# Performance work log

Hardware: AMD Instinct MI355X
Metric: run time of the kernel (lower is better)

## Reference

```python
import jax, jax.numpy as jnp
import numpy as np

B, N, QD = 2, 4096, 512
HEADS, DIM_HEAD = 8, 64
INNER = HEADS * DIM_HEAD  # 512
SCALE = DIM_HEAD ** -0.5


def setup_inputs() -> dict:
    key = jax.random.key(0)
    ks = jax.random.split(key, 6)
    s = 0.02
    return {
        "x": jax.random.normal(ks[0], (B, N, QD), dtype=jnp.float32),
        "Wq": jax.random.normal(ks[1], (QD, INNER), dtype=jnp.float32) * s,
        "Wk": jax.random.normal(ks[2], (QD, INNER), dtype=jnp.float32) * s,
        "Wv": jax.random.normal(ks[3], (QD, INNER), dtype=jnp.float32) * s,
        "Wo": jax.random.normal(ks[4], (INNER, QD), dtype=jnp.float32) * s,
        "bo": jnp.zeros((QD,), dtype=jnp.float32),
    }


def reference(x, Wq, Wk, Wv, Wo, bo):
    # self-attention: context = x; mask = None; attention_sf = False
    q = x @ Wq  # [B, N, INNER]
    k = x @ Wk
    v = x @ Wv
    # split heads: [B, H, N, D]
    def split(t):
        return t.reshape(B, N, HEADS, DIM_HEAD).transpose(0, 2, 1, 3)
    q, k, v = split(q), split(k), split(v)
    # fp32 QK^T (ATTN_PRECISION='fp32' path)
    sim = jnp.einsum('bhid,bhjd->bhij', q.astype(jnp.float32), k.astype(jnp.float32)) * SCALE
    attn = jax.nn.softmax(sim, axis=-1)
    out = jnp.einsum('bhij,bhjd->bhid', attn, v)  # [B, H, N, D]
    out = out.transpose(0, 2, 1, 3).reshape(B, N, INNER)
    return out @ Wo + bo  # Dropout(p=0) is identity
```

## Files before the change

### kernel.cpp

```cpp
#include <hip/hip_runtime.h>
#include <hip/hip_bf16.h>


typedef __attribute__((ext_vector_type(8))) short short8;
typedef __attribute__((ext_vector_type(4))) float floatx4;

#define MFMA16(a, b, c) __builtin_amdgcn_mfma_f32_16x16x32_bf16((a), (b), (c), 0, 0, 0)

static __device__ __forceinline__ unsigned short f2b(float f) {
  unsigned int u = __float_as_uint(f);
  u += 0x7FFFu + ((u >> 16) & 1u);
  return (unsigned short)(u >> 16);
}

static __device__ __forceinline__ unsigned int pkb(float a, float b) {
  float2 t{a, b};
  __hip_bfloat162 h = __float22bfloat162_rn(t);
  union { __hip_bfloat162 h2; unsigned int u; } cv;
  cv.h2 = h;
  return cv.u;
}

__global__ __launch_bounds__(256) void wt_cvt_kernel(
    const float* __restrict__ Wq, const float* __restrict__ Wk,
    const float* __restrict__ Wv, const float* __restrict__ Wo,
    unsigned short* __restrict__ wtq, unsigned short* __restrict__ wtk,
    unsigned short* __restrict__ wtv, unsigned short* __restrict__ wto) {
  const int z = blockIdx.z;
  const float* __restrict__ W = (z == 0) ? Wq : (z == 1) ? Wk : (z == 2) ? Wv : Wo;
  unsigned short* __restrict__ T = (z == 0) ? wtq : (z == 1) ? wtk : (z == 2) ? wtv : wto;
  const int k0 = blockIdx.x * 32, c0 = blockIdx.y * 32;
  __shared__ float Ts[32][33];
  const int tid = threadIdx.x;
  const int r = tid >> 3, cc = (tid & 7) * 4;
  const float4 v = *(const float4*)(W + (k0 + r) * 512 + c0 + cc);
  Ts[r][cc] = v.x; Ts[r][cc + 1] = v.y; Ts[r][cc + 2] = v.z; Ts[r][cc + 3] = v.w;
  __syncthreads();
  const unsigned long long uu =
      (unsigned long long)pkb(Ts[cc][r], Ts[cc + 1][r]) |
      ((unsigned long long)pkb(Ts[cc + 2][r], Ts[cc + 3][r]) << 32);
  *(unsigned long long*)(T + (c0 + r) * 512 + k0 + cc) = uu;
}

__global__ __launch_bounds__(256) void qkv_proj_kernel(
    const float* __restrict__ x, const unsigned short* __restrict__ wtq,
    const unsigned short* __restrict__ wtk,
    const unsigned short* __restrict__ wtv, unsigned short* __restrict__ qo,
    unsigned short* __restrict__ ko, unsigned short* __restrict__ vo) {
  const int z = blockIdx.z;
  const unsigned short* __restrict__ wt = (z == 0) ? wtq : (z == 1) ? wtk : wtv;
  const int m0 = blockIdx.x * 128;
  const int c0 = blockIdx.y * 128;
  __shared__ __align__(16) unsigned short As[128 * 40];
  __shared__ __align__(16) unsigned short Bs[128 * 40];
  const int tid = threadIdx.x;
  const int lane = tid & 63, wvid = tid >> 6;
  const int i = lane & 15, q = lane >> 4;
  const int wy = wvid >> 1, wx = wvid & 1;
  const int arow = tid >> 1, ch = (tid & 1) * 16;
  floatx4 acc[4][4] = {};
  for (int k0 = 0; k0 < 512; k0 += 32) {
    __syncthreads();
    {
      const float* src = x + (m0 + arow) * 512 + k0 + ch;
      unsigned int av[8];
#pragma unroll
      for (int j = 0; j < 8; ++j) av[j] = pkb(src[2 * j], src[2 * j + 1]);
      *(short8*)&As[arow * 40 + ch] = *(short8*)&av[0];
      *(short8*)&As[arow * 40 + ch + 8] = *(short8*)&av[4];
      const unsigned short* bs = wt + (c0 + arow) * 512 + k0 + ch;
      *(short8*)&Bs[arow * 40 + ch] = *(const short8*)(bs);
      *(short8*)&Bs[arow * 40 + ch + 8] = *(const short8*)(bs + 8);
    }
    __syncthreads();
    short8 af[4], bfr[4];
#pragma unroll
    for (int t = 0; t < 4; ++t)
      af[t] = *(const short8*)&As[(wy * 64 + t * 16 + i) * 40 + q * 8];
#pragma unroll
    for (int g = 0; g < 4; ++g)
      bfr[g] = *(const short8*)&Bs[(wx * 64 + g * 16 + i) * 40 + q * 8];
#pragma unroll
    for (int t = 0; t < 4; ++t)
#pragma unroll
      for (int g = 0; g < 4; ++g) acc[t][g] = MFMA16(af[t], bfr[g], acc[t][g]);
  }
#pragma unroll
  for (int t = 0; t < 4; ++t)
#pragma unroll
    for (int g = 0; g < 4; ++g) {
      const int col = c0 + wx * 64 + g * 16 + i;
      const int h = col >> 6, d = col & 63;
      const int row0 = m0 + wy * 64 + t * 16 + q * 4;
      const int b = row0 >> 12;
      const int n0 = row0 & 4095;
      if (z == 2) {
        unsigned int* dst =
            (unsigned int*)&vo[(((b * 8 + h) * 64 + d) << 12) + n0];
        dst[0] = pkb(acc[t][g][0], acc[t][g][1]);
        dst[1] = pkb(acc[t][g][2], acc[t][g][3]);
      } else {
        unsigned short* dst = (z == 0) ? qo : ko;
        const float sc = (z == 0) ? 0.125f : 1.0f;
#pragma unroll
        for (int r = 0; r < 4; ++r)
          dst[(((b * 8 + h) << 12) + (n0 + r)) * 64 + d] =
              f2b(acc[t][g][r] * sc);
      }
    }
}

__global__ __launch_bounds__(256, 4) void flash_kernel(
    const unsigned short* __restrict__ Q, const unsigned short* __restrict__ K,
    const unsigned short* __restrict__ Vt, unsigned short* __restrict__ O) {
  const int bh = blockIdx.x;
  const int m0 = blockIdx.y * 128;
  const int tid = threadIdx.x;
  const int lane = tid & 63, w = tid >> 6;
  const int i = lane & 15, q = lane >> 4;
  const unsigned short* qp = Q + bh * (4096 * 64);
  const unsigned short* kp = K + bh * (4096 * 64);
  const unsigned short* vp = Vt + bh * (64 * 4096);

  __shared__ __align__(16) unsigned short Ks[64 * 72];
  __shared__ __align__(16) unsigned short Vs[64 * 72];
  __shared__ __align__(16) unsigned short Ps[4][32 * 72];

  const int srow = tid >> 3;
  const int scol = (tid & 7) * 8;
  const unsigned short* kg = kp + srow * 64 + scol;
  const unsigned short* vg = vp + srow * 4096 + scol;

  short8 qf[2][2];
#pragma unroll
  for (int t = 0; t < 2; ++t)
#pragma unroll
    for (int kc = 0; kc < 2; ++kc)
      qf[t][kc] = *(const short8*)(qp + (m0 + w * 32 + t * 16 + i) * 64 +
                                   kc * 32 + q * 8);

  floatx4 accO[2][4] = {};
  floatx4 accL[2] = {};
  short8 ones;
  {
    const short ov = (i == 0) ? (short)0x3F80 : (short)0;
#pragma unroll
    for (int j = 0; j < 8; ++j) ones[j] = ov;
  }
  const floatx4 zf = {0.f, 0.f, 0.f, 0.f};

  *(short8*)&Ks[srow * 72 + scol] = *(const short8*)(kg);
  *(short8*)&Ks[(srow + 32) * 72 + scol] = *(const short8*)(kg + 32 * 64);
  *(short8*)&Vs[srow * 72 + scol] = *(const short8*)(vg);
  *(short8*)&Vs[(srow + 32) * 72 + scol] = *(const short8*)(vg + 32 * 4096);
  __syncthreads();

  unsigned short* pw = &Ps[w][0];
  for (int jt = 0; jt < 64; ++jt) {
    short8 kn0, kn1, vn0, vn1;
    if (jt < 63) {
      kn0 = *(const short8*)(kg + (jt + 1) * 4096);
      kn1 = *(const short8*)(kg + (jt + 1) * 4096 + 32 * 64);
      vn0 = *(const short8*)(vg + (jt + 1) * 64);
      vn1 = *(const short8*)(vg + (jt + 1) * 64 + 32 * 4096);
    }
#pragma unroll
    for (int g = 0; g < 4; ++g) {
      const short8 kf0 = *(const short8*)(&Ks[(g * 16 + i) * 72 + q * 8]);
      const short8 kf1 = *(const short8*)(&Ks[(g * 16 + i) * 72 + 32 + q * 8]);
#pragma unroll
      for (int t = 0; t < 2; ++t) {
        floatx4 s = MFMA16(kf0, qf[t][0], zf);
        s = MFMA16(kf1, qf[t][1], s);
        const float e0 = __expf(s[0]), e1 = __expf(s[1]);
        const float e2 = __expf(s[2]), e3 = __expf(s[3]);
        *(unsigned long long*)&pw[(t * 16 + i) * 72 + g * 16 + q * 4] =
            (unsigned long long)pkb(e0, e1) |
            ((unsigned long long)pkb(e2, e3) << 32);
      }
    }
    short8 pf[2][2];
#pragma unroll
    for (int t = 0; t < 2; ++t) {
      pf[t][0] = *(const short8*)(pw + (t * 16 + i) * 72 + q * 8);
      pf[t][1] = *(const short8*)(pw + (t * 16 + i) * 72 + 32 + q * 8);
      accL[t] = MFMA16(pf[t][0], ones, accL[t]);
      accL[t] = MFMA16(pf[t][1], ones, accL[t]);
    }
#pragma unroll
    for (int dg = 0; dg < 4; ++dg) {
      const short8 vf0 = *(const short8*)(&Vs[(dg * 16 + i) * 72 + q * 8]);
      const short8 vf1 = *(const short8*)(&Vs[(dg * 16 + i) * 72 + 32 + q * 8]);
#pragma unroll
      for (int t = 0; t < 2; ++t) {
        accO[t][dg] = MFMA16(pf[t][0], vf0, accO[t][dg]);
        accO[t][dg] = MFMA16(pf[t][1], vf1, accO[t][dg]);
      }
    }
    __syncthreads();
    if (jt < 63) {
      *(short8*)&Ks[srow * 72 + scol] = kn0;
      *(short8*)&Ks[(srow + 32) * 72 + scol] = kn1;
      *(short8*)&Vs[srow * 72 + scol] = vn0;
      *(short8*)&Vs[(srow + 32) * 72 + scol] = vn1;
    }
    __syncthreads();
  }

  const int b = bh >> 3, h = bh & 7;
#pragma unroll
  for (int t = 0; t < 2; ++t) {
    float inv[4];
#pragma unroll
    for (int r = 0; r < 4; ++r) {
      const float l = __shfl(accL[t][r], lane & 48, 64);
      inv[r] = 1.0f / l;
    }
#pragma unroll
    for (int dg = 0; dg < 4; ++dg)
#pragma unroll
      for (int r = 0; r < 4; ++r) {
        const int n = m0 + w * 32 + t * 16 + q * 4 + r;
        const int col = h * 64 + dg * 16 + i;
        O[((b << 12) + n) * 512 + col] = f2b(accO[t][dg][r] * inv[r]);
      }
  }
}

__global__ __launch_bounds__(256) void out_proj_kernel(
    const unsigned short* __restrict__ A, const unsigned short* __restrict__ wto,
    const float* __restrict__ bo, float* __restrict__ out) {
  const int m0 = blockIdx.x * 128, c0 = blockIdx.y * 128;
  __shared__ __align__(16) unsigned short As[128 * 40];
  __shared__ __align__(16) unsigned short Bs[128 * 40];
  const int tid = threadIdx.x;
  const int lane = tid & 63, wvid = tid >> 6;
  const int i = lane & 15, q = lane >> 4;
  const int wy = wvid >> 1, wx = wvid & 1;
  const int arow = tid >> 1, ch = (tid & 1) * 16;
  floatx4 acc[4][4] = {};
  for (int k0 = 0; k0 < 512; k0 += 32) {
    __syncthreads();
    {
      const unsigned short* as = A + (m0 + arow) * 512 + k0 + ch;
      *(short8*)&As[arow * 40 + ch] = *(const short8*)(as);
      *(short8*)&As[arow * 40 + ch + 8] = *(const short8*)(as + 8);
      const unsigned short* bs = wto + (c0 + arow) * 512 + k0 + ch;
      *(short8*)&Bs[arow * 40 + ch] = *(const short8*)(bs);
      *(short8*)&Bs[arow * 40 + ch + 8] = *(const short8*)(bs + 8);
    }
    __syncthreads();
    short8 af[4], bfr[4];
#pragma unroll
    for (int t = 0; t < 4; ++t)
      af[t] = *(const short8*)&As[(wy * 64 + t * 16 + i) * 40 + q * 8];
#pragma unroll
    for (int g = 0; g < 4; ++g)
      bfr[g] = *(const short8*)&Bs[(wx * 64 + g * 16 + i) * 40 + q * 8];
#pragma unroll
    for (int t = 0; t < 4; ++t)
#pragma unroll
      for (int g = 0; g < 4; ++g) acc[t][g] = MFMA16(af[t], bfr[g], acc[t][g]);
  }
#pragma unroll
  for (int t = 0; t < 4; ++t)
#pragma unroll
    for (int g = 0; g < 4; ++g) {
      const int col = c0 + wx * 64 + g * 16 + i;
      const float bias = bo[col];
#pragma unroll
      for (int r = 0; r < 4; ++r) {
        const int row = m0 + wy * 64 + t * 16 + q * 4 + r;
        out[row * 512 + col] = acc[t][g][r] + bias;
      }
    }
}

extern "C" void kernel_launch(void* const* d_in, const int* in_sizes, int n_in,
                              void* d_out, int out_size, void* d_ws,
                              size_t ws_size, hipStream_t stream) {
  const float* x = (const float*)d_in[0];
  const float* Wq = (const float*)d_in[1];
  const float* Wk = (const float*)d_in[2];
  const float* Wv = (const float*)d_in[3];
  const float* Wo = (const float*)d_in[4];
  const float* bo = (const float*)d_in[5];
  float* out = (float*)d_out;

  const size_t tsz = (size_t)16 * 4096 * 64;
  unsigned short* qws = (unsigned short*)d_ws;
  unsigned short* kws = qws + tsz;
  unsigned short* vws = kws + tsz;
  unsigned short* ows = vws + tsz;
  unsigned short* wtq = ows + tsz;
  unsigned short* wtk = wtq + 512 * 512;
  unsigned short* wtv = wtk + 512 * 512;
  unsigned short* wto = wtv + 512 * 512;

  wt_cvt_kernel<<<dim3(16, 16, 4), 256, 0, stream>>>(Wq, Wk, Wv, Wo, wtq, wtk,
                                                     wtv, wto);
  qkv_proj_kernel<<<dim3(64, 4, 3), 256, 0, stream>>>(x, wtq, wtk, wtv, qws,
                                                      kws, vws);
  flash_kernel<<<dim3(16, 32), 256, 0, stream>>>(qws, kws, vws, ows);
  out_proj_kernel<<<dim3(64, 4), 256, 0, stream>>>(ows, wto, bo, out);
}
```

Before: 225.5 us.

## Split flash KV range across wave pairs, swizzle LDS, use exp2, shrink out-proj tiles

The flash kernel now takes 64-row query tiles, with pairs of waves splitting each 64-key block into two 32-key halves. The two partial outputs and row sums are combined through shared memory at the end, which doubles the grid and raises occupancy. LDS tiles use XOR swizzles in place of padding, and exp is replaced by exp2 with log2(e) folded into the Q scale. Row sums move from an MFMA with a ones vector to scalar adds plus shuffles. The output projection switches to 64x64 tiles for more blocks, at the cost of less data reuse per tile.

Result: slower. 239.1 us (+6.1%).

```diff
diff --git a/kernel.cpp b/kernel.cpp
--- a/kernel.cpp
+++ b/kernel.cpp
@@ -6,6 +6,14 @@
 typedef __attribute__((ext_vector_type(4))) float floatx4;
 
 #define MFMA16(a, b, c) __builtin_amdgcn_mfma_f32_16x16x32_bf16((a), (b), (c), 0, 0, 0)
+
+#if __has_builtin(__builtin_amdgcn_exp2f)
+#define EXP2(x) __builtin_amdgcn_exp2f(x)
+#else
+#define EXP2(x) exp2f(x)
+#endif
+
+#define QSCALE 0.18033688011112042f
 
 static __device__ __forceinline__ unsigned short f2b(float f) {
   unsigned int u = __float_as_uint(f);
@@ -101,7 +109,7 @@
         dst[1] = pkb(acc[t][g][2], acc[t][g][3]);
       } else {
         unsigned short* dst = (z == 0) ? qo : ko;
-        const float sc = (z == 0) ? 0.125f : 1.0f;
+        const float sc = (z == 0) ? QSCALE : 1.0f;
 #pragma unroll
         for (int r = 0; r < 4; ++r)
           dst[(((b * 8 + h) << 12) + (n0 + r)) * 64 + d] =
@@ -110,101 +118,132 @@
     }
 }
 
-__global__ __launch_bounds__(256, 4) void flash_kernel(
+__global__ __launch_bounds__(256, 5) void flash_kernel(
     const unsigned short* __restrict__ Q, const unsigned short* __restrict__ K,
     const unsigned short* __restrict__ Vt, unsigned short* __restrict__ O) {
-  const int bh = blockIdx.x;
-  const int m0 = blockIdx.y * 128;
+  const int m0 = blockIdx.x * 64;
+  const int bh = blockIdx.y;
   const int tid = threadIdx.x;
   const int lane = tid & 63, w = tid >> 6;
   const int i = lane & 15, q = lane >> 4;
+  const int rt = w & 1;
+  const int kg = w >> 1;
+  const int sl7 = i & 7, sl3 = i & 3;
   const unsigned short* qp = Q + bh * (4096 * 64);
   const unsigned short* kp = K + bh * (4096 * 64);
   const unsigned short* vp = Vt + bh * (64 * 4096);
 
-  __shared__ __align__(16) unsigned short Ks[64 * 72];
-  __shared__ __align__(16) unsigned short Vs[64 * 72];
-  __shared__ __align__(16) unsigned short Ps[4][32 * 72];
-
-  const int srow = tid >> 3;
-  const int scol = (tid & 7) * 8;
-  const unsigned short* kg = kp + srow * 64 + scol;
-  const unsigned short* vg = vp + srow * 4096 + scol;
+  __shared__ __align__(16) unsigned short SM[12288];
+  unsigned short* Ks = SM + kg * 2048;
+  unsigned short* Vs = SM + 4096 + kg * 2048;
+  unsigned short* pw = SM + 8192 + w * 1024;
+
+  const int t128 = tid & 127;
+  const int sr = t128 >> 2;
+  const int sc = t128 & 3;
+  const unsigned short* kgl = kp + (kg * 2048 + sr) * 64 + sc * 8;
+  const int ko1 = sr * 64 + ((sc ^ (sr & 7)) * 8);
+  const int ko2 = sr * 64 + (((sc + 4) ^ (sr & 7)) * 8);
+  const unsigned short* vgl = vp + sr * 4096 + kg * 2048 + sc * 8;
+  const int vo1 = sr * 32 + ((sc ^ (sr & 3)) * 8);
+  const int vo2 = (sr + 32) * 32 + ((sc ^ (sr & 3)) * 8);
 
   short8 qf[2][2];
 #pragma unroll
   for (int t = 0; t < 2; ++t)
 #pragma unroll
     for (int kc = 0; kc < 2; ++kc)
-      qf[t][kc] = *(const short8*)(qp + (m0 + w * 32 + t * 16 + i) * 64 +
+      qf[t][kc] = *(const short8*)(qp + (m0 + rt * 32 + t * 16 + i) * 64 +
                                    kc * 32 + q * 8);
 
   floatx4 accO[2][4] = {};
-  floatx4 accL[2] = {};
-  short8 ones;
-  {
-    const short ov = (i == 0) ? (short)0x3F80 : (short)0;
-#pragma unroll
-    for (int j = 0; j < 8; ++j) ones[j] = ov;
-  }
+  float Lacc[2] = {0.f, 0.f};
   const floatx4 zf = {0.f, 0.f, 0.f, 0.f};
 
-  *(short8*)&Ks[srow * 72 + scol] = *(const short8*)(kg);
-  *(short8*)&Ks[(srow + 32) * 72 + scol] = *(const short8*)(kg + 32 * 64);
-  *(short8*)&Vs[srow * 72 + scol] = *(const short8*)(vg);
-  *(short8*)&Vs[(srow + 32) * 72 + scol] = *(const short8*)(vg + 32 * 4096);
+  *(short8*)&Ks[ko1] = *(const short8*)(kgl);
+  *(short8*)&Ks[ko2] = *(const short8*)(kgl + 32);
+  *(short8*)&Vs[vo1] = *(const short8*)(vgl);
+  *(short8*)&Vs[vo2] = *(const short8*)(vgl + 32 * 4096);
   __syncthreads();
 
-  unsigned short* pw = &Ps[w][0];
   for (int jt = 0; jt < 64; ++jt) {
-    short8 kn0, kn1, vn0, vn1;
-    if (jt < 63) {
-      kn0 = *(const short8*)(kg + (jt + 1) * 4096);
-      kn1 = *(const short8*)(kg + (jt + 1) * 4096 + 32 * 64);
-      vn0 = *(const short8*)(vg + (jt + 1) * 64);
-      vn1 = *(const short8*)(vg + (jt + 1) * 64 + 32 * 4096);
-    }
-#pragma unroll
-    for (int g = 0; g < 4; ++g) {
-      const short8 kf0 = *(const short8*)(&Ks[(g * 16 + i) * 72 + q * 8]);
-      const short8 kf1 = *(const short8*)(&Ks[(g * 16 + i) * 72 + 32 + q * 8]);
+#pragma unroll
+    for (int g = 0; g < 2; ++g) {
+      const short8 kf0 =
+          *(const short8*)&Ks[(g * 16 + i) * 64 + ((q ^ sl7) * 8)];
+      const short8 kf1 =
+          *(const short8*)&Ks[(g * 16 + i) * 64 + (((4 + q) ^ sl7) * 8)];
 #pragma unroll
       for (int t = 0; t < 2; ++t) {
         floatx4 s = MFMA16(kf0, qf[t][0], zf);
         s = MFMA16(kf1, qf[t][1], s);
-        const float e0 = __expf(s[0]), e1 = __expf(s[1]);
-        const float e2 = __expf(s[2]), e3 = __expf(s[3]);
-        *(unsigned long long*)&pw[(t * 16 + i) * 72 + g * 16 + q * 4] =
+        const float e0 = EXP2(s[0]), e1 = EXP2(s[1]);
+        const float e2 = EXP2(s[2]), e3 = EXP2(s[3]);
+        Lacc[t] += (e0 + e1) + (e2 + e3);
+        *(unsigned long long*)&pw[(t * 16 + i) * 32 +
+                                  (((2 * g + (q >> 1)) ^ sl3) * 8) +
+                                  (q & 1) * 4] =
             (unsigned long long)pkb(e0, e1) |
             ((unsigned long long)pkb(e2, e3) << 32);
       }
     }
-    short8 pf[2][2];
+    short8 pf[2];
+#pragma unroll
+    for (int t = 0; t < 2; ++t)
+      pf[t] = *(const short8*)&pw[(t * 16 + i) * 32 + ((q ^ sl3) * 8)];
+#pragma unroll
+    for (int dg = 0; dg < 4; ++dg) {
+      const short8 vfd =
+          *(const short8*)&Vs[(dg * 16 + i) * 32 + ((q ^ sl3) * 8)];
+      accO[0][dg] = MFMA16(pf[0], vfd, accO[0][dg]);
+      accO[1][dg] = MFMA16(pf[1], vfd, accO[1][dg]);
+    }
+    short8 kn0, kn1, vn0, vn1;
+    if (jt < 63) {
+      kn0 = *(const short8*)(kgl + (jt + 1) * 2048);
+      kn1 = *(const short8*)(kgl + (jt + 1) * 2048 + 32);
+      vn0 = *(const short8*)(vgl + (jt + 1) * 32);
+      vn1 = *(const short8*)(vgl + (jt + 1) * 32 + 32 * 4096);
+    }
+    __syncthreads();
+    if (jt < 63) {
+      *(short8*)&Ks[ko1] = kn0;
+      *(short8*)&Ks[ko2] = kn1;
+      *(short8*)&Vs[vo1] = vn0;
+      *(short8*)&Vs[vo2] = vn1;
+    }
+    __syncthreads();
+  }
+
+#pragma unroll
+  for (int t = 0; t < 2; ++t) {
+    Lacc[t] += __shfl_xor(Lacc[t], 16);
+    Lacc[t] += __shfl_xor(Lacc[t], 32);
+  }
+  float* MB = (float*)SM;
+  if (kg == 1) {
+    float* dst = MB + (rt * 64 + lane) * 35;
 #pragma unroll
     for (int t = 0; t < 2; ++t) {
-      pf[t][0] = *(const short8*)(pw + (t * 16 + i) * 72 + q * 8);
-      pf[t][1] = *(const short8*)(pw + (t * 16 + i) * 72 + 32 + q * 8);
-      accL[t] = MFMA16(pf[t][0], ones, accL[t]);
-      accL[t] = MFMA16(pf[t][1], ones, accL[t]);
-    }
-#pragma unroll
-    for (int dg = 0; dg < 4; ++dg) {
-      const short8 vf0 = *(const short8*)(&Vs[(dg * 16 + i) * 72 + q * 8]);
-      const short8 vf1 = *(const short8*)(&Vs[(dg * 16 + i) * 72 + 32 + q * 8]);
-#pragma unroll
-      for (int t = 0; t < 2; ++t) {
-        accO[t][dg] = MFMA16(pf[t][0], vf0, accO[t][dg]);
-        accO[t][dg] = MFMA16(pf[t][1], vf1, accO[t][dg]);
-      }
-    }
-    __syncthreads();
-    if (jt < 63) {
-      *(short8*)&Ks[srow * 72 + scol] = kn0;
-      *(short8*)&Ks[(srow + 32) * 72 + scol] = kn1;
-      *(short8*)&Vs[srow * 72 + scol] = vn0;
-      *(short8*)&Vs[(srow + 32) * 72 + scol] = vn1;
-    }
-    __syncthreads();
+#pragma unroll
+      for (int dg = 0; dg < 4; ++dg)
+#pragma unroll
+        for (int r = 0; r < 4; ++r) dst[t * 16 + dg * 4 + r] = accO[t][dg][r];
+      dst[32 + t] = Lacc[t];
+    }
+  }
+  __syncthreads();
+  if (kg == 1) return;
+  {
+    const float* src = MB + (rt * 64 + lane) * 35;
+#pragma unroll
+    for (int t = 0; t < 2; ++t) {
+#pragma unroll
+      for (int dg = 0; dg < 4; ++dg)
+#pragma unroll
+        for (int r = 0; r < 4; ++r) accO[t][dg][r] += src[t * 16 + dg * 4 + r];
+      Lacc[t] += src[32 + t];
+    }
   }
 
   const int b = bh >> 3, h = bh & 7;
@@ -213,14 +252,14 @@
     float inv[4];
 #pragma unroll
     for (int r = 0; r < 4; ++r) {
-      const float l = __shfl(accL[t][r], lane & 48, 64);
+      const float l = __shfl(Lacc[t], (lane & 48) | ((lane >> 4) * 4 + r), 64);
       inv[r] = 1.0f / l;
     }
 #pragma unroll
     for (int dg = 0; dg < 4; ++dg)
 #pragma unroll
       for (int r = 0; r < 4; ++r) {
-        const int n = m0 + w * 32 + t * 16 + q * 4 + r;
+        const int n = m0 + rt * 32 + t * 16 + q * 4 + r;
         const int col = h * 64 + dg * 16 + i;
         O[((b << 12) + n) * 512 + col] = f2b(accO[t][dg][r] * inv[r]);
       }
@@ -230,47 +269,43 @@
 __global__ __launch_bounds__(256) void out_proj_kernel(
     const unsigned short* __restrict__ A, const unsigned short* __restrict__ wto,
     const float* __restrict__ bo, float* __restrict__ out) {
-  const int m0 = blockIdx.x * 128, c0 = blockIdx.y * 128;
-  __shared__ __align__(16) unsigned short As[128 * 40];
-  __shared__ __align__(16) unsigned short Bs[128 * 40];
+  const int m0 = blockIdx.x * 64, c0 = blockIdx.y * 64;
+  __shared__ __align__(16) unsigned short As[64 * 40];
+  __shared__ __align__(16) unsigned short Bs[64 * 40];
   const int tid = threadIdx.x;
   const int lane = tid & 63, wvid = tid >> 6;
   const int i = lane & 15, q = lane >> 4;
   const int wy = wvid >> 1, wx = wvid & 1;
-  const int arow = tid >> 1, ch = (tid & 1) * 16;
-  floatx4 acc[4][4] = {};
+  const int arow = tid >> 2, acol = (tid & 3) * 8;
+  floatx4 acc[2][2] = {};
   for (int k0 = 0; k0 < 512; k0 += 32) {
     __syncthreads();
-    {
-      const unsigned short* as = A + (m0 + arow) * 512 + k0 + ch;
-      *(short8*)&As[arow * 40 + ch] = *(const short8*)(as);
-      *(short8*)&As[arow * 40 + ch + 8] = *(const short8*)(as + 8);
-      const unsigned short* bs = wto + (c0 + arow) * 512 + k0 + ch;
-      *(short8*)&Bs[arow * 40 + ch] = *(const short8*)(bs);
-      *(short8*)&Bs[arow * 40 + ch + 8] = *(const short8*)(bs + 8);
-    }
-    __syncthreads();
-    short8 af[4], bfr[4];
-#pragma unroll
-    for (int t = 0; t < 4; ++t)
-      af[t] = *(const short8*)&As[(wy * 64 + t * 16 + i) * 40 + q * 8];
-#pragma unroll
-    for (int g = 0; g < 4; ++g)
-      bfr[g] = *(const short8*)&Bs[(wx * 64 + g * 16 + i) * 40 + q * 8];
-#pragma unroll
-    for (int t = 0; t < 4; ++t)
-#pragma unroll
-      for (int g = 0; g < 4; ++g) acc[t][g] = MFMA16(af[t], bfr[g], acc[t][g]);
-  }
-#pragma unroll
-  for (int t = 0; t < 4; ++t)
-#pragma unroll
-    for (int g = 0; g < 4; ++g) {
-      const int col = c0 + wx * 64 + g * 16 + i;
+    *(short8*)&As[arow * 40 + acol] =
+        *(const short8*)(A + (m0 + arow) * 512 + k0 + acol);
+    *(short8*)&Bs[arow * 40 + acol] =
+        *(const short8*)(wto + (c0 + arow) * 512 + k0 + acol);
+    __syncthreads();
+    short8 af[2], bfr[2];
+#pragma unroll
+    for (int t = 0; t < 2; ++t)
+      af[t] = *(const short8*)&As[(wy * 32 + t * 16 + i) * 40 + q * 8];
+#pragma unroll
+    for (int g = 0; g < 2; ++g)
+      bfr[g] = *(const short8*)&Bs[(wx * 32 + g * 16 + i) * 40 + q * 8];
+#pragma unroll
+    for (int t = 0; t < 2; ++t)
+#pragma unroll
+      for (int g = 0; g < 2; ++g) acc[t][g] = MFMA16(af[t], bfr[g], acc[t][g]);
+  }
+#pragma unroll
+  for (int t = 0; t < 2; ++t)
+#pragma unroll
+    for (int g = 0; g < 2; ++g) {
+      const int col = c0 + wx * 32 + g * 16 + i;
       const float bias = bo[col];
 #pragma unroll
       for (int r = 0; r < 4; ++r) {
-        const int row = m0 + wy * 64 + t * 16 + q * 4 + r;
+        const int row = m0 + wy * 32 + t * 16 + q * 4 + r;
         out[row * 512 + col] = acc[t][g][r] + bias;
       }
     }
@@ -301,6 +336,6 @@
                                                      wtv, wto);
   qkv_proj_kernel<<<dim3(64, 4, 3), 256, 0, stream>>>(x, wtq, wtk, wtv, qws,
                                                       kws, vws);
-  flash_kernel<<<dim3(16, 32), 256, 0, stream>>>(qws, kws, vws, ows);
-  out_proj_kernel<<<dim3(64, 4), 256, 0, stream>>>(ows, wto, bo, out);
-}
+  flash_kernel<<<dim3(64, 16), 256, 0, stream>>>(qws, kws, vws, ows);
+  out_proj_kernel<<<dim3(128, 8), 256, 0, stream>>>(ows, wto, bo, out);
+}
```
